# Performance work log

Hardware: AMD Instinct MI355X
Metric: run time of the kernel (lower is better)

Reference implementation:

```python
import jax, jax.numpy as jnp
import numpy as np

THETA = 10000.0
NUM_HEADS = 16


def _rope(x, positions):
    # x: [B, H, S, Dk] (fp32), positions: [B, S] int
    d_k = x.shape[-1]
    k = jnp.arange(0, d_k, 2, dtype=jnp.float32)
    freqs = THETA ** (-k / d_k)                      # [Dk/2]
    angles = positions[..., None].astype(jnp.float32) * freqs  # [B, S, Dk/2]
    cos = jnp.cos(angles)[:, None, :, :]             # [B, 1, S, Dk/2]
    sin = jnp.sin(angles)[:, None, :, :]
    xr = x.reshape(*x.shape[:-1], d_k // 2, 2)
    x_even, x_odd = xr[..., 0], xr[..., 1]
    rot_even = x_even * cos - x_odd * sin
    rot_odd = x_even * sin + x_odd * cos
    out = jnp.stack([rot_even, rot_odd], axis=-1)
    return out.reshape(x.shape)


def setup_inputs() -> dict:
    key = jax.random.key(0)
    ks = jax.random.split(key, 6)
    B, S, D = 2, 2048, 1024
    std = (2.0 / (D + D)) ** 0.5
    x = jax.random.normal(ks[0], (B, S, D), dtype=jnp.float32)
    Wq = jax.random.normal(ks[1], (D, D), dtype=jnp.float32) * std
    Wk = jax.random.normal(ks[2], (D, D), dtype=jnp.float32) * std
    Wv = jax.random.normal(ks[3], (D, D), dtype=jnp.float32) * std
    Wo = jax.random.normal(ks[4], (D, D), dtype=jnp.float32) * std
    token_positions = jnp.broadcast_to(jnp.arange(S, dtype=jnp.int32), (B, S))
    return {"x": x, "Wq": Wq, "Wk": Wk, "Wv": Wv, "Wo": Wo,
            "token_positions": token_positions}


def reference(x, Wq, Wk, Wv, Wo, token_positions):
    B, S, D = x.shape
    H = NUM_HEADS
    Dk = D // H
    # QKV projections (no bias): y = x @ W.T
    def proj(W):
        return (x @ W.T).reshape(B, S, H, Dk).transpose(0, 2, 1, 3)  # [B,H,S,Dk]
    Q, K, V = proj(Wq), proj(Wk), proj(Wv)
    Q = _rope(Q, token_positions)
    K = _rope(K, token_positions)
    scale = 1.0 / jnp.sqrt(jnp.float32(Dk))
    scores = jnp.einsum('bhqd,bhkd->bhqk', Q, K) * scale  # [B,H,S,S]
    causal = jnp.tril(jnp.ones((S, S), dtype=bool))
    scores = jnp.where(causal, scores, -jnp.inf)
    attn = jax.nn.softmax(scores.astype(jnp.float32), axis=-1)
    out = jnp.einsum('bhqk,bhkd->bhqd', attn, V)          # [B,H,S,Dk]
    out = out.transpose(0, 2, 1, 3).reshape(B, S, D)
    return out @ Wo.T
```

## Files before the change

### kernel.cpp

```cpp
#include <hip/hip_runtime.h>
#include <math.h>

#define D_MODEL 1024
#define NHEADS 16
#define DK 64
#define SEQ 2048
#define BATCH 2
#define MROWS (BATCH * SEQ)

typedef __attribute__((ext_vector_type(8))) short bfrag8;
typedef __attribute__((ext_vector_type(4))) float f32x4;
typedef unsigned short u16;
typedef __attribute__((ext_vector_type(8))) u16 u16x8;
typedef __attribute__((ext_vector_type(4))) u16 u16x4;

#define GLOBAL_AS(p) ((const __attribute__((address_space(1))) void*)(p))
#define LDS_AS(p)    ((__attribute__((address_space(3))) void*)(p))

__device__ inline u16 f2bf(float f) {
  union { float f; unsigned u; } c; c.f = f;
  unsigned r = c.u + 0x7FFF + ((c.u >> 16) & 1);
  return (u16)(r >> 16);
}

__device__ inline unsigned pack_bf2(float lo, float hi) {
  return __builtin_amdgcn_perm(__float_as_uint(hi), __float_as_uint(lo), 0x07060302);
}

__global__ __launch_bounds__(256)
void build_rope_tab(const int* __restrict__ pos, float2* __restrict__ tab) {
  int idx = blockIdx.x * 256 + threadIdx.x;
  int i = idx & 31, bs = idx >> 5;
  float p = (float)pos[bs];
  float freq = expf(-(float)i * 0.2878231366242558f);
  float sn, cs;
  sincosf(p * freq, &sn, &cs);
  tab[idx] = make_float2(cs, sn);
}

struct CvtPtrs { const float* src[5]; };

__global__ __launch_bounds__(256)
void convert_inputs(CvtPtrs p, u16* __restrict__ dst) {
  size_t base = ((size_t)blockIdx.x * 256 + threadIdx.x) * 4;
  const size_t XSZ = (size_t)MROWS * D_MODEL;
  const float* s; size_t off;
  if (base < XSZ) { s = p.src[0]; off = base; }
  else {
    size_t j = base - XSZ;
    s = p.src[1 + (int)(j >> 20)];
    off = j & ((1u << 20) - 1);
  }
  float4 v = *(const float4*)(s + off);
  u16 o[4] = { f2bf(v.x), f2bf(v.y), f2bf(v.z), f2bf(v.w) };
  *(u16x4*)(dst + base) = *(u16x4*)o;
}

__device__ inline void gemm_core(const u16* __restrict__ A, const u16* __restrict__ B,
                                 int m0, int n0, u16* As, u16* Bs,
                                 f32x4 acc[4][4]) {
  const int tid = threadIdx.x;
  const int w = tid >> 6, lane = tid & 63;
  const int l15 = lane & 15, quad = lane >> 4;
  const int wm = w >> 1, wn = w & 1;
  const int srow = tid >> 2;
  const int scol = (tid & 3) * 8;

  #pragma unroll
  for (int mi = 0; mi < 4; ++mi)
    #pragma unroll
    for (int ni = 0; ni < 4; ++ni) acc[mi][ni] = (f32x4)0.f;

  for (int k0 = 0; k0 < D_MODEL; k0 += 32) {
    __syncthreads();
    #pragma unroll
    for (int i = 0; i < 2; ++i) {
      const u16* ga = A + (size_t)((i * 64 + srow) + m0) * D_MODEL + k0 + scol;
      const u16* gb = B + (size_t)((i * 64 + srow) + n0) * D_MODEL + k0 + scol;
      __builtin_amdgcn_global_load_lds(GLOBAL_AS(ga), LDS_AS(&As[(i * 64 + w * 16) * 32]), 16, 0, 0);
      __builtin_amdgcn_global_load_lds(GLOBAL_AS(gb), LDS_AS(&Bs[(i * 64 + w * 16) * 32]), 16, 0, 0);
    }
    __syncthreads();

    bfrag8 af[4], bfr[4];
    #pragma unroll
    for (int i = 0; i < 4; ++i) {
      af[i]  = *(const bfrag8*)&As[(wm * 64 + i * 16 + l15) * 32 + quad * 8];
      bfr[i] = *(const bfrag8*)&Bs[(wn * 64 + i * 16 + l15) * 32 + quad * 8];
    }
    #pragma unroll
    for (int mi = 0; mi < 4; ++mi)
      #pragma unroll
      for (int ni = 0; ni < 4; ++ni)
        acc[mi][ni] = __builtin_amdgcn_mfma_f32_16x16x32_bf16(af[mi], bfr[ni], acc[mi][ni], 0, 0, 0);
  }
}

struct QKVArgs { const u16* A[3]; const u16* B[3]; u16* dst[3]; const float2* tab; };

__global__ __launch_bounds__(256)
void gemm_qkv_fused(QKVArgs p) {
  __shared__ u16 As[128 * 32];
  __shared__ u16 Bs[128 * 32];
  const int z = blockIdx.z;
  const int bi = blockIdx.x;
  int m0, n0;
  if (z < 2) { m0 = (bi & 7) * 128; n0 = (bi >> 3) * 128; }
  else       { m0 = (bi >> 3) * 128; n0 = (bi & 7) * 128; }
  f32x4 acc[4][4];
  gemm_core(p.A[z], p.B[z], m0, n0, As, Bs, acc);

  const int tid = threadIdx.x;
  const int w = tid >> 6, lane = tid & 63;
  const int l15 = lane & 15, quad = lane >> 4;
  const int wm = w >> 1, wn = w & 1;
  u16* dst = p.dst[z];

  if (z < 2) {
    const int head = (m0 + wm * 64) >> 6;
    const float scale = (z == 0) ? 0.125f * 1.4426950408889634f : 1.0f;
    #pragma unroll
    for (int ni = 0; ni < 4; ++ni) {
      int sg = n0 + wn * 64 + ni * 16 + l15;
      int b = sg >> 11;
      int s = sg & (SEQ - 1);
      size_t ho = ((size_t)(b * NHEADS + head)) * SEQ * DK;
      #pragma unroll
      for (int mi = 0; mi < 4; ++mi) {
        float4 t = *(const float4*)&p.tab[(size_t)sg * 32 + mi * 8 + quad * 2];
        float e0 = acc[mi][ni][0], o0 = acc[mi][ni][1];
        float e1 = acc[mi][ni][2], o1 = acc[mi][ni][3];
        u16x4 ov = { f2bf((e0 * t.x - o0 * t.y) * scale),
                     f2bf((e0 * t.y + o0 * t.x) * scale),
                     f2bf((e1 * t.z - o1 * t.w) * scale),
                     f2bf((e1 * t.w + o1 * t.z) * scale) };
        *(u16x4*)&dst[ho + (size_t)s * DK + mi * 16 + quad * 4] = ov;
      }
    }
  } else {
    const int b = m0 >> 11;
    const int head = (n0 >> 6) + wn;
    const size_t ho = ((size_t)(b * NHEADS + head)) * SEQ * DK;
    const int row_base = m0 + wm * 64;
    #pragma unroll
    for (int mi = 0; mi < 4; ++mi)
      #pragma unroll
      for (int ni = 0; ni < 4; ++ni) {
        int d = ni * 16 + l15;
        int sb = (row_base + mi * 16 + quad * 4) & (SEQ - 1);
        u16 o[4];
        #pragma unroll
        for (int r = 0; r < 4; ++r) o[r] = f2bf(acc[mi][ni][r]);
        *(u16x4*)&dst[ho + (size_t)d * SEQ + sb] = *(u16x4*)o;
      }
  }
}

__global__ __launch_bounds__(256)
void gemm_out_bf16(const u16* __restrict__ A, const u16* __restrict__ B,
                   float* __restrict__ C) {
  __shared__ u16 As[128 * 32];
  __shared__ u16 Bs[64 * 32];
  const int m0 = blockIdx.y * 128, n0 = blockIdx.x * 64;
  const int tid = threadIdx.x;
  const int w = tid >> 6, lane = tid & 63;
  const int l15 = lane & 15, quad = lane >> 4;
  const int wm = w >> 1, wn = w & 1;
  const int lrow = lane >> 2;
  const int lcol = (lane & 3) * 8;

  f32x4 acc[4][2];
  #pragma unroll
  for (int mi = 0; mi < 4; ++mi)
    #pragma unroll
    for (int ni = 0; ni < 2; ++ni) acc[mi][ni] = (f32x4)0.f;

  for (int k0 = 0; k0 < D_MODEL; k0 += 32) {
    __syncthreads();
    #pragma unroll
    for (int i = 0; i < 2; ++i) {
      int row = (i * 4 + w) * 16 + lrow;
      const u16* ga = A + (size_t)(m0 + row) * D_MODEL + k0 + lcol;
      __builtin_amdgcn_global_load_lds(GLOBAL_AS(ga), LDS_AS(&As[(i * 4 + w) * 16 * 32]), 16, 0, 0);
    }
    {
      int row = w * 16 + lrow;
      const u16* gb = B + (size_t)(n0 + row) * D_MODEL + k0 + lcol;
      __builtin_amdgcn_global_load_lds(GLOBAL_AS(gb), LDS_AS(&Bs[w * 16 * 32]), 16, 0, 0);
    }
    __syncthreads();

    bfrag8 af[4], bfr[2];
    #pragma unroll
    for (int i = 0; i < 4; ++i)
      af[i] = *(const bfrag8*)&As[(wm * 64 + i * 16 + l15) * 32 + quad * 8];
    #pragma unroll
    for (int i = 0; i < 2; ++i)
      bfr[i] = *(const bfrag8*)&Bs[(wn * 32 + i * 16 + l15) * 32 + quad * 8];
    #pragma unroll
    for (int mi = 0; mi < 4; ++mi)
      #pragma unroll
      for (int ni = 0; ni < 2; ++ni)
        acc[mi][ni] = __builtin_amdgcn_mfma_f32_16x16x32_bf16(af[mi], bfr[ni], acc[mi][ni], 0, 0, 0);
  }

  #pragma unroll
  for (int mi = 0; mi < 4; ++mi)
    #pragma unroll
    for (int ni = 0; ni < 2; ++ni)
      #pragma unroll
      for (int r = 0; r < 4; ++r) {
        int row = m0 + wm * 64 + mi * 16 + quad * 4 + r;
        int col = n0 + wn * 32 + ni * 16 + l15;
        C[(size_t)row * D_MODEL + col] = acc[mi][ni][r];
      }
}

#define PSTR 72

__global__ __launch_bounds__(512)
void attn_mfma(const u16* __restrict__ Qbf, const u16* __restrict__ Kbf,
               const u16* __restrict__ Vtb, u16* __restrict__ obb) {
  __shared__ u16 Ks[64 * 64];
  __shared__ u16 Vt[64 * 64];
  __shared__ u16 Ps[8][16 * PSTR];

  const int tid = threadIdx.x;
  const int w = tid >> 6, lane = tid & 63;
  const int l15 = lane & 15, quad = lane >> 4;
  const int hb = blockIdx.x >> 4;
  const int qp = blockIdx.x & 15;
  const int qt = (w < 4) ? qp : (31 - qp);
  const int b = hb >> 4, h = hb & 15;
  const size_t ho = (size_t)hb * SEQ * DK;
  const int qrow_base = qt * 64 + (w & 3) * 16;

  bfrag8 qf[2];
  #pragma unroll
  for (int hh = 0; hh < 2; ++hh)
    qf[hh] = *(const bfrag8*)&Qbf[ho + (size_t)(qrow_base + l15) * DK + hh * 32 + quad * 8];

  f32x4 oacc[4];
  float m_ = -1e30f, l_ = 0.f;
  #pragma unroll
  for (int n0 = 0; n0 < 4; ++n0) oacc[n0] = (f32x4)0.f;

  const int srow = w * 8 + (lane >> 3);
  const int scc = ((lane & 7) ^ (srow & 7)) * 8;

  const int ntiles = 32 - qp;
  for (int t = 0; t < ntiles; ++t) {
    const int j0 = t * 64;
    __syncthreads();
    __builtin_amdgcn_global_load_lds(GLOBAL_AS(Kbf + ho + (size_t)(j0 + srow) * DK + scc),
                                     LDS_AS(&Ks[w * 512]), 16, 0, 0);
    __builtin_amdgcn_global_load_lds(GLOBAL_AS(Vtb + ho + (size_t)srow * SEQ + j0 + scc),
                                     LDS_AS(&Vt[w * 512]), 16, 0, 0);
    __syncthreads();

    if (t > qt) continue;

    f32x4 sc[4];
    #pragma unroll
    for (int st = 0; st < 4; ++st) {
      int key = st * 16 + l15;
      int sw = l15 & 7;
      bfrag8 kf0 = *(const bfrag8*)&Ks[key * 64 + ((quad ^ sw) * 8)];
      bfrag8 kf1 = *(const bfrag8*)&Ks[key * 64 + (((4 + quad) ^ sw) * 8)];
      sc[st] = __builtin_amdgcn_mfma_f32_16x16x32_bf16(kf0, qf[0], (f32x4)0.f, 0, 0, 0);
      sc[st] = __builtin_amdgcn_mfma_f32_16x16x32_bf16(kf1, qf[1], sc[st], 0, 0, 0);
    }

    if (j0 + 63 > qrow_base) {
      #pragma unroll
      for (int st = 0; st < 4; ++st)
        #pragma unroll
        for (int r = 0; r < 4; ++r) {
          int key = j0 + st * 16 + quad * 4 + r;
          if (key > qrow_base + l15) sc[st][r] = -1e30f;
        }
    }

    float mx = sc[0][0];
    #pragma unroll
    for (int st = 0; st < 4; ++st)
      #pragma unroll
      for (int r = 0; r < 4; ++r) mx = fmaxf(mx, sc[st][r]);
    mx = fmaxf(mx, __shfl_xor(mx, 16));
    mx = fmaxf(mx, __shfl_xor(mx, 32));
    float mnew = fmaxf(m_, mx);
    float alpha = __builtin_amdgcn_exp2f(m_ - mnew);
    m_ = mnew;
    float pv[4][4], rs = 0.f;
    #pragma unroll
    for (int st = 0; st < 4; ++st)
      #pragma unroll
      for (int r = 0; r < 4; ++r) {
        pv[st][r] = __builtin_amdgcn_exp2f(sc[st][r] - mnew);
        rs += pv[st][r];
      }
    rs += __shfl_xor(rs, 16);
    rs += __shfl_xor(rs, 32);
    l_ = l_ * alpha + rs;
    #pragma unroll
    for (int n0 = 0; n0 < 4; ++n0) oacc[n0] *= alpha;

    #pragma unroll
    for (int st = 0; st < 4; ++st) {
      uint2 pk = { pack_bf2(pv[st][0], pv[st][1]), pack_bf2(pv[st][2], pv[st][3]) };
      *(uint2*)&Ps[w][l15 * PSTR + st * 16 + quad * 4] = pk;
    }
    __asm__ volatile("s_waitcnt lgkmcnt(0)" ::: "memory");

    bfrag8 pf[2];
    #pragma unroll
    for (int kc = 0; kc < 2; ++kc)
      pf[kc] = *(const bfrag8*)&Ps[w][l15 * PSTR + kc * 32 + quad * 8];
    #pragma unroll
    for (int n0 = 0; n0 < 4; ++n0) {
      int sw = l15 & 7;
      #pragma unroll
      for (int kc = 0; kc < 2; ++kc) {
        bfrag8 vf = *(const bfrag8*)&Vt[(n0 * 16 + l15) * 64 + (((kc * 4 + quad) ^ sw) * 8)];
        oacc[n0] = __builtin_amdgcn_mfma_f32_16x16x32_bf16(vf, pf[kc], oacc[n0], 0, 0, 0);
      }
    }
  }

  float inv = 1.f / l_;
  int q = qrow_base + l15;
  #pragma unroll
  for (int n0 = 0; n0 < 4; ++n0) {
    u16x4 ov = { f2bf(oacc[n0][0] * inv), f2bf(oacc[n0][1] * inv),
                 f2bf(oacc[n0][2] * inv), f2bf(oacc[n0][3] * inv) };
    *(u16x4*)&obb[(size_t)(b * SEQ + q) * D_MODEL + h * DK + n0 * 16 + quad * 4] = ov;
  }
}

extern "C" void kernel_launch(void* const* d_in, const int* in_sizes, int n_in,
                              void* d_out, int out_size, void* d_ws, size_t ws_size,
                              hipStream_t stream) {
  const float* x  = (const float*)d_in[0];
  const float* Wq = (const float*)d_in[1];
  const float* Wk = (const float*)d_in[2];
  const float* Wv = (const float*)d_in[3];
  const float* Wo = (const float*)d_in[4];
  const int* pos  = (const int*)d_in[5];

  const size_t XSZ = (size_t)MROWS * D_MODEL;
  const size_t WSZ = (size_t)D_MODEL * D_MODEL;

  u16* bfb = (u16*)d_ws;
  u16* xb  = bfb;
  u16* wqb = xb  + XSZ;
  u16* wkb = wqb + WSZ;
  u16* wvb = wkb + WSZ;
  u16* wob = wvb + WSZ;
  u16* Qbf = wob + WSZ;
  u16* Kbf = Qbf + XSZ;
  u16* Vtb = Kbf + XSZ;
  u16* obb = Vtb + XSZ;
  float2* tab = (float2*)(obb + XSZ);

  build_rope_tab<<<(BATCH * SEQ * 32) / 256, 256, 0, stream>>>(pos, tab);

  CvtPtrs cp; cp.src[0] = x; cp.src[1] = Wq; cp.src[2] = Wk; cp.src[3] = Wv; cp.src[4] = Wo;
  size_t cvtElems = XSZ + 4 * WSZ;
  convert_inputs<<<(int)(cvtElems / 4 / 256), 256, 0, stream>>>(cp, xb);

  QKVArgs qp;
  qp.A[0] = wqb; qp.A[1] = wkb; qp.A[2] = xb;
  qp.B[0] = xb;  qp.B[1] = xb;  qp.B[2] = wvb;
  qp.dst[0] = Qbf; qp.dst[1] = Kbf; qp.dst[2] = Vtb;
  qp.tab = tab;
  gemm_qkv_fused<<<dim3(256, 1, 3), 256, 0, stream>>>(qp);

  attn_mfma<<<dim3(512), 512, 0, stream>>>(Qbf, Kbf, Vtb, obb);

  gemm_out_bf16<<<dim3(D_MODEL / 64, MROWS / 128), 256, 0, stream>>>(obb, wob, (float*)d_out);
}
```

Measured before the change: 192.9 us.

## Double-buffer K/V tiles in attention kernel with async prefetch

The attention kernel now keeps two LDS buffers for the K and V^T tiles. The next tile is issued via global_load_lds before the current one is computed, with raw s_barrier and vmcnt waits replacing __syncthreads. This hides global load latency behind MFMA work, at the cost of doubling K/V LDS usage, which may reduce occupancy. It also relies on hand-tuned waitcnt ordering being correct.

```diff
diff --git a/kernel.cpp b/kernel.cpp
--- a/kernel.cpp
+++ b/kernel.cpp
@@ -16,6 +16,10 @@
 
 #define GLOBAL_AS(p) ((const __attribute__((address_space(1))) void*)(p))
 #define LDS_AS(p)    ((__attribute__((address_space(3))) void*)(p))
+
+#define RAW_BARRIER()  __asm__ volatile("s_barrier" ::: "memory")
+#define WAIT_VM2()     __asm__ volatile("s_waitcnt vmcnt(2)" ::: "memory")
+#define WAIT_VM0()     __asm__ volatile("s_waitcnt vmcnt(0)" ::: "memory")
 
 __device__ inline u16 f2bf(float f) {
   union { float f; unsigned u; } c; c.f = f;
@@ -221,8 +225,8 @@
 __global__ __launch_bounds__(512)
 void attn_mfma(const u16* __restrict__ Qbf, const u16* __restrict__ Kbf,
                const u16* __restrict__ Vtb, u16* __restrict__ obb) {
-  __shared__ u16 Ks[64 * 64];
-  __shared__ u16 Vt[64 * 64];
+  __shared__ u16 Ks[2][64 * 64];
+  __shared__ u16 Vt[2][64 * 64];
   __shared__ u16 Ps[8][16 * PSTR];
 
   const int tid = threadIdx.x;
@@ -248,15 +252,28 @@
   const int srow = w * 8 + (lane >> 3);
   const int scc = ((lane & 7) ^ (srow & 7)) * 8;
 
+  #define STAGE(T, BUF) do {                                                         \
+    int j0_ = (T) * 64;                                                              \
+    __builtin_amdgcn_global_load_lds(GLOBAL_AS(Kbf + ho + (size_t)(j0_ + srow) * DK + scc), \
+                                     LDS_AS(&Ks[BUF][w * 512]), 16, 0, 0);           \
+    __builtin_amdgcn_global_load_lds(GLOBAL_AS(Vtb + ho + (size_t)srow * SEQ + j0_ + scc), \
+                                     LDS_AS(&Vt[BUF][w * 512]), 16, 0, 0);           \
+  } while (0)
+
   const int ntiles = 32 - qp;
+  STAGE(0, 0);
+
   for (int t = 0; t < ntiles; ++t) {
     const int j0 = t * 64;
-    __syncthreads();
-    __builtin_amdgcn_global_load_lds(GLOBAL_AS(Kbf + ho + (size_t)(j0 + srow) * DK + scc),
-                                     LDS_AS(&Ks[w * 512]), 16, 0, 0);
-    __builtin_amdgcn_global_load_lds(GLOBAL_AS(Vtb + ho + (size_t)srow * SEQ + j0 + scc),
-                                     LDS_AS(&Vt[w * 512]), 16, 0, 0);
-    __syncthreads();
+    const int buf = t & 1;
+    RAW_BARRIER();
+    if (t + 1 < ntiles) {
+      STAGE(t + 1, buf ^ 1);
+      WAIT_VM2();
+    } else {
+      WAIT_VM0();
+    }
+    RAW_BARRIER();
 
     if (t > qt) continue;
 
@@ -265,8 +282,8 @@
     for (int st = 0; st < 4; ++st) {
       int key = st * 16 + l15;
       int sw = l15 & 7;
-      bfrag8 kf0 = *(const bfrag8*)&Ks[key * 64 + ((quad ^ sw) * 8)];
-      bfrag8 kf1 = *(const bfrag8*)&Ks[key * 64 + (((4 + quad) ^ sw) * 8)];
+      bfrag8 kf0 = *(const bfrag8*)&Ks[buf][key * 64 + ((quad ^ sw) * 8)];
+      bfrag8 kf1 = *(const bfrag8*)&Ks[buf][key * 64 + (((4 + quad) ^ sw) * 8)];
       sc[st] = __builtin_amdgcn_mfma_f32_16x16x32_bf16(kf0, qf[0], (f32x4)0.f, 0, 0, 0);
       sc[st] = __builtin_amdgcn_mfma_f32_16x16x32_bf16(kf1, qf[1], sc[st], 0, 0, 0);
     }
@@ -321,11 +338,12 @@
       int sw = l15 & 7;
       #pragma unroll
       for (int kc = 0; kc < 2; ++kc) {
-        bfrag8 vf = *(const bfrag8*)&Vt[(n0 * 16 + l15) * 64 + (((kc * 4 + quad) ^ sw) * 8)];
+        bfrag8 vf = *(const bfrag8*)&Vt[buf][(n0 * 16 + l15) * 64 + (((kc * 4 + quad) ^ sw) * 8)];
         oacc[n0] = __builtin_amdgcn_mfma_f32_16x16x32_bf16(vf, pf[kc], oacc[n0], 0, 0, 0);
       }
     }
   }
+  #undef STAGE
 
   float inv = 1.f / l_;
   int q = qrow_base + l15;
```

After: 192.3 us. No clear change (-0.4%).
